# Performance work log

Measured on AMD Instinct MI355X. Metric: run time of the kernel, lower is better.

## Reference

```python
import jax, jax.numpy as jnp
import numpy as np

CH = 16        # channel_n
HID = 128      # hidden_size
IN_CH = 3      # input_channels (locked each step)
FIRE_RATE = 0.5


def _dwconv3x3(x, w, b):
    # depthwise 3x3, reflect padding (torch padding_mode='reflect', padding=1)
    xp = jnp.pad(x, ((0, 0), (0, 0), (1, 1), (1, 1)), mode='reflect')
    y = jax.lax.conv_general_dilated(
        xp, w, window_strides=(1, 1), padding='VALID',
        dimension_numbers=('NCHW', 'OIHW', 'NCHW'), feature_group_count=CH)
    return y + b[None, :, None, None]


def _conv1x1(x, w, b=None):
    # w: (out_ch, in_ch) -- squeezed 1x1 conv kernel
    y = jnp.einsum('bchw,oc->bohw', x, w)
    return y if b is None else y + b[None, :, None, None]


def setup_inputs() -> dict:
    key = jax.random.key(0)
    ks = jax.random.split(key, 8)
    B, H, W = 4, 256, 256
    x = jax.random.normal(ks[0], (B, CH, H, W), dtype=jnp.float32)
    # depthwise kernels: (CH, 1, 3, 3)
    p0_w = jax.random.normal(ks[1], (CH, 1, 3, 3), dtype=jnp.float32) * (1.0 / 3.0)
    p0_b = jax.random.normal(ks[2], (CH,), dtype=jnp.float32) * 0.1
    p1_w = jax.random.normal(ks[3], (CH, 1, 3, 3), dtype=jnp.float32) * (1.0 / 3.0)
    p1_b = jax.random.normal(ks[4], (CH,), dtype=jnp.float32) * 0.1
    # fc0: Conv2d(3*CH -> HID, k=1); fc1: Conv2d(HID -> CH, k=1, bias=False)
    fc0_w = jax.random.normal(ks[5], (HID, 3 * CH), dtype=jnp.float32) * (1.0 / np.sqrt(3 * CH))
    fc0_b = jax.random.normal(ks[6], (HID,), dtype=jnp.float32) * 0.1
    # NOTE: torch zero-inits fc1; we use small random weights so the reference is non-trivial.
    fc1_w = jax.random.normal(ks[7], (CH, HID), dtype=jnp.float32) * (0.1 / np.sqrt(HID))
    return {"x": x, "p0_w": p0_w, "p0_b": p0_b, "p1_w": p1_w, "p1_b": p1_b,
            "fc0_w": fc0_w, "fc0_b": fc0_b, "fc1_w": fc1_w, "steps": 32}


def reference(x, p0_w, p0_b, p1_w, p1_b, fc0_w, fc0_b, fc1_w, steps):
    B, _, H, W = x.shape
    input_image = x[:, :IN_CH]  # clone of input channels, re-written each step
    keys = jax.random.split(jax.random.key(42), steps)

    @jax.checkpoint
    def step(x, key):
        # perceive: depthwise 3x3 x2, concat with state
        z1 = _dwconv3x3(x, p0_w, p0_b)
        z2 = _dwconv3x3(x, p1_w, p1_b)
        y = jnp.concatenate([x, z1, z2], axis=1)        # [B, 3*CH, H, W]
        # 1x1-conv MLP
        dx = jax.nn.relu(_conv1x1(y, fc0_w, fc0_b))      # [B, HID, H, W]
        dx = _conv1x1(dx, fc1_w)                         # [B, CH, H, W]
        # stochastic fire mask: rand > fire_rate, broadcast over channels
        mask = (jax.random.uniform(key, (B, 1, H, W), dtype=x.dtype) > FIRE_RATE).astype(x.dtype)
        x = x + dx * mask                                # residual update
        x = x.at[:, :IN_CH].set(input_image)             # channel lock
        return x, None

    x, _ = jax.lax.scan(step, x, keys)
    out = x[:, 3]  # segmentation channel
    return out, x
```

## Files before the change

### kernel.cpp

```cpp
#include <hip/hip_runtime.h>
#include <cstdint>

#define CH     16
#define HPIX   256
#define WPIX   256
#define BATCH  4
#define HID    128
#define STEPS  32
#define PLANE  (HPIX * WPIX)
#define MASK_N (BATCH * PLANE)

#define TW 32
#define TH 8
#define XTW 34
#define XTH 10
#define NPX (XTH * XTW)
#define HSF 20

typedef _Float16 half8  __attribute__((ext_vector_type(8)));
typedef _Float16 half4e __attribute__((ext_vector_type(4)));
typedef float floatx4  __attribute__((ext_vector_type(4)));
typedef float floatx16 __attribute__((ext_vector_type(16)));

__host__ __device__ static inline void tf2x32(uint32_t k0, uint32_t k1,
                                              uint32_t x0, uint32_t x1,
                                              uint32_t& o0, uint32_t& o1) {
  const uint32_t ks2 = k0 ^ k1 ^ 0x1BD11BDAu;
#define TFROT(a) { x0 += x1; x1 = (x1 << (a)) | (x1 >> (32 - (a))); x1 ^= x0; }
  x0 += k0;  x1 += k1;
  TFROT(13) TFROT(15) TFROT(26) TFROT(6)
  x0 += k1;  x1 += ks2 + 1u;
  TFROT(17) TFROT(29) TFROT(16) TFROT(24)
  x0 += ks2; x1 += k0 + 2u;
  TFROT(13) TFROT(15) TFROT(26) TFROT(6)
  x0 += k0;  x1 += k1 + 3u;
  TFROT(17) TFROT(29) TFROT(16) TFROT(24)
  x0 += k1;  x1 += ks2 + 4u;
  TFROT(13) TFROT(15) TFROT(26) TFROT(6)
  x0 += ks2; x1 += k0 + 5u;
#undef TFROT
  o0 = x0; o1 = x1;
}

__global__ __launch_bounds__(256) void prep_weights(
    const float* __restrict__ fc0_w, const float* __restrict__ fc0_b,
    const float* __restrict__ fc1_w,
    const float* __restrict__ p0_w, const float* __restrict__ p0_b,
    const float* __restrict__ p1_w, const float* __restrict__ p1_b,
    _Float16* __restrict__ Mh, _Float16* __restrict__ W1h,
    float* __restrict__ bp) {
  const int idx = blockIdx.x * 256 + threadIdx.x;
  if (idx < 9 * HID * CH) {
    const int tap = idx / (HID * CH);
    const int rem = idx - tap * (HID * CH);
    const int h = rem >> 4, c = rem & 15;
    float m = fc0_w[h * 48 + 16 + c] * p0_w[c * 9 + tap]
            + fc0_w[h * 48 + 32 + c] * p1_w[c * 9 + tap];
    if (tap == 4) m += fc0_w[h * 48 + c];
    Mh[(tap * HID + h) * CH + c] = (_Float16)m;
  } else if (idx < 9 * HID * CH + CH * HID) {
    const int i2 = idx - 9 * HID * CH;
    W1h[i2] = (_Float16)fc1_w[i2];
  } else if (idx < 9 * HID * CH + CH * HID + HID) {
    const int h = idx - (9 * HID * CH + CH * HID);
    float s = fc0_b[h];
    for (int c = 0; c < CH; ++c)
      s += fc0_w[h * 48 + 16 + c] * p0_b[c]
         + fc0_w[h * 48 + 32 + c] * p1_b[c];
    bp[h] = s;
  }
}

__global__ __launch_bounds__(256) void nca_step(
    const float* __restrict__ x_in, float* __restrict__ x_out,
    const float* __restrict__ x0,
    const _Float16* __restrict__ Mh, const _Float16* __restrict__ W1h,
    const float* __restrict__ bp,
    uint32_t k0, uint32_t k1, int wrgb, float* __restrict__ outp) {
  __shared__ __align__(16) _Float16 halo[NPX * HSF];
  __shared__ __align__(16) _Float16 Hbuf[64 * HID];
  __shared__ float maskbuf[TW * TH];

  const int tid = threadIdx.x;
  const int w0 = blockIdx.x * TW;
  const int h0 = blockIdx.y * TH;
  const int b  = blockIdx.z;

  const int wv   = tid >> 6;
  const int lane = tid & 63;
  const int n    = lane & 15;
  const int g    = lane >> 4;
  const int c32  = lane & 31;
  const int q2   = lane >> 5;

  const float* __restrict__ xb  = x_in + (size_t)b * CH * PLANE;
  const float* __restrict__ x0b = x0   + (size_t)b * CH * PLANE;

  half8 Atap[9];
  #pragma unroll
  for (int t = 0; t < 9; ++t)
    Atap[t] = *(const half8*)(Mh + ((t * HID + 32 * wv + c32) << 4) + 8 * q2);
  half8 bw1[4];
  #pragma unroll
  for (int s = 0; s < 4; ++s)
    bw1[s] = *(const half8*)(W1h + n * HID + 32 * s + 8 * g);
  float4 bias4[4];
  #pragma unroll
  for (int rb = 0; rb < 4; ++rb)
    bias4[rb] = *(const float4*)(bp + 32 * wv + 8 * rb + 4 * q2);

  float4 xcv[4];
  size_t xoff[4];
  #pragma unroll
  for (int k = 0; k < 4; ++k) {
    xoff[k] = (size_t)n * PLANE
            + (size_t)(h0 + 2 * k + (wv >> 1)) * WPIX
            + w0 + 16 * (wv & 1) + 4 * g;
    xcv[k] = *(const float4*)(((n < 3) ? x0b : xb) + xoff[k]);
  }

  for (int t = tid; t < NPX; t += 256) {
    const int hr = t / XTW, hc = t - (t / XTW) * XTW;
    int gh = h0 + hr - 1;
    gh = (gh < 0) ? -gh : ((gh > HPIX - 1) ? (2 * (HPIX - 1) - gh) : gh);
    int gw = w0 + hc - 1;
    gw = (gw < 0) ? -gw : ((gw > WPIX - 1) ? (2 * (WPIX - 1) - gw) : gw);
    const float* __restrict__ srcS = xb  + gh * WPIX + gw;
    const float* __restrict__ src0 = x0b + gh * WPIX + gw;
    #pragma unroll
    for (int blk = 0; blk < 4; ++blk) {
      half4e h4;
      #pragma unroll
      for (int e = 0; e < 4; ++e) {
        const int c = 4 * blk + e;
        h4[e] = (_Float16)((c < 3 ? src0 : srcS)[(size_t)c * PLANE]);
      }
      *(half4e*)(halo + t * HSF + 4 * blk) = h4;
    }
  }

  {
    const int hp = h0 + (tid >> 5), wp = w0 + (tid & 31);
    const uint32_t j = (uint32_t)(b * PLANE + hp * WPIX + wp);
    uint32_t r0, r1;
    tf2x32(k0, k1, 0u, j, r0, r1);
    const uint32_t bits = r0 ^ r1;
    union { uint32_t i; float f; } cvt;
    cvt.i = (bits >> 9) | 0x3F800000u;
    maskbuf[tid] = ((cvt.f - 1.0f) > 0.5f) ? 1.0f : 0.0f;
  }
  __syncthreads();

  float* __restrict__ xob = x_out + (size_t)b * CH * PLANE;

  #pragma unroll
  for (int k = 0; k < 4; ++k) {
    #pragma unroll
    for (int cti = 0; cti < 2; ++cti) {
      const int ct = 2 * k + cti;
      half8 btap[9];
      #pragma unroll
      for (int dr = 0; dr < 3; ++dr) {
        #pragma unroll
        for (int dj = 0; dj < 3; ++dj) {
          const _Float16* hp =
              halo + ((ct + dr) * XTW + c32 + dj) * HSF + 8 * q2;
          const half4e lo = *(const half4e*)hp;
          const half4e hi = *(const half4e*)(hp + 4);
          half8 ff;
          ff[0] = lo[0]; ff[1] = lo[1]; ff[2] = lo[2]; ff[3] = lo[3];
          ff[4] = hi[0]; ff[5] = hi[1]; ff[6] = hi[2]; ff[7] = hi[3];
          btap[dr * 3 + dj] = ff;
        }
      }
      floatx16 acc = {0.f,0.f,0.f,0.f,0.f,0.f,0.f,0.f,
                      0.f,0.f,0.f,0.f,0.f,0.f,0.f,0.f};
      #pragma unroll
      for (int t = 0; t < 9; ++t)
        acc = __builtin_amdgcn_mfma_f32_32x32x16_f16(Atap[t], btap[t], acc,
                                                     0, 0, 0);
      const int ph  = 32 * cti + c32;
      const int n16 = c32 & 15;
      #pragma unroll
      for (int rb = 0; rb < 4; ++rb) {
        half4e hv;
        hv[0] = (_Float16)fmaxf(acc[4 * rb + 0] + bias4[rb].x, 0.f);
        hv[1] = (_Float16)fmaxf(acc[4 * rb + 1] + bias4[rb].y, 0.f);
        hv[2] = (_Float16)fmaxf(acc[4 * rb + 2] + bias4[rb].z, 0.f);
        hv[3] = (_Float16)fmaxf(acc[4 * rb + 3] + bias4[rb].w, 0.f);
        *(half4e*)(Hbuf + ph * HID + (((4 * wv + rb) ^ n16) << 3) + 4 * q2) = hv;
      }
    }
    __syncthreads();

    {
      floatx4 c2 = {0.f, 0.f, 0.f, 0.f};
      #pragma unroll
      for (int ks = 0; ks < 4; ++ks) {
        const half8 a2 = *(const half8*)(
            Hbuf + (16 * wv + n) * HID + (((4 * ks + g) ^ n) << 3));
        c2 = __builtin_amdgcn_mfma_f32_16x16x32_f16(a2, bw1[ks], c2, 0, 0, 0);
      }
      const int prow = 2 * k + (wv >> 1);
      const int pcol = 16 * (wv & 1) + 4 * g;
      const float4 mk = *(const float4*)(maskbuf + prow * TW + pcol);
      const float4 xc = xcv[k];
      float4 res;
      res.x = (n < 3) ? xc.x : fmaf(mk.x, c2[0], xc.x);
      res.y = (n < 3) ? xc.y : fmaf(mk.y, c2[1], xc.y);
      res.z = (n < 3) ? xc.z : fmaf(mk.z, c2[2], xc.z);
      res.w = (n < 3) ? xc.w : fmaf(mk.w, c2[3], xc.w);
      if (n >= 3 || wrgb)
        *(float4*)(xob + xoff[k]) = res;
      if (wrgb && n == 3) {
        *(float4*)(outp + (size_t)b * PLANE
                   + (size_t)(h0 + prow) * WPIX + w0 + pcol) = res;
      }
    }
    if (k < 3) __syncthreads();
  }
}

extern "C" void kernel_launch(void* const* d_in, const int* in_sizes, int n_in,
                              void* d_out, int out_size, void* d_ws, size_t ws_size,
                              hipStream_t stream) {
  const float* x     = (const float*)d_in[0];
  const float* p0_w  = (const float*)d_in[1];
  const float* p0_b  = (const float*)d_in[2];
  const float* p1_w  = (const float*)d_in[3];
  const float* p1_b  = (const float*)d_in[4];
  const float* fc0_w = (const float*)d_in[5];
  const float* fc0_b = (const float*)d_in[6];
  const float* fc1_w = (const float*)d_in[7];

  uint32_t kk[STEPS][2];
  for (int i = 0; i < STEPS; ++i) {
    uint32_t a, b2;
    tf2x32(0u, 42u, 0u, (uint32_t)i, a, b2);
    kk[i][0] = a;
    kk[i][1] = b2;
  }

  float* out = (float*)d_out;
  float* bufA = out + MASK_N;
  float* bufB = (float*)d_ws;

  _Float16* Mh  = (_Float16*)((char*)d_ws + ((size_t)32 << 20));
  _Float16* W1h = Mh + 9 * HID * CH;
  float*    bpr = (float*)((char*)W1h + CH * HID * 2);

  const int prep_n = 9 * HID * CH + CH * HID + HID;
  prep_weights<<<dim3((prep_n + 255) / 256), dim3(256), 0, stream>>>(
      fc0_w, fc0_b, fc1_w, p0_w, p0_b, p1_w, p1_b, Mh, W1h, bpr);

  const dim3 grid(WPIX / TW, HPIX / TH, BATCH);
  const dim3 block(256);

  for (int i = 0; i < STEPS; ++i) {
    const float* src = (i == 0) ? x : ((i & 1) ? bufB : bufA);
    float* dst = (i & 1) ? bufA : bufB;
    nca_step<<<grid, block, 0, stream>>>(src, dst, x, Mh, W1h, bpr,
                                         kk[i][0], kk[i][1],
                                         (i == STEPS - 1) ? 1 : 0, out);
  }
}
```

Before: 759.4 us.

## Fuse two NCA steps per launch using halo recomputation

Each kernel launch now advances two NCA steps. It loads a 2-pixel halo frame, computes the step-1 update for the interior tile and also recomputes it on a 1-pixel rim, then runs step 2 from shared memory. The tile width is halved to 16, and reflect-padding fixups are applied at image borders. This halves the number of launches and the global memory round trips of the state. In exchange it adds redundant rim computation of about 52 extra pixels per 128, more barriers, and more shared memory.

```diff
diff --git a/kernel.cpp b/kernel.cpp
--- a/kernel.cpp
+++ b/kernel.cpp
@@ -7,15 +7,17 @@
 #define BATCH  4
 #define HID    128
 #define STEPS  32
+#define NPAIR  (STEPS / 2)
 #define PLANE  (HPIX * WPIX)
 #define MASK_N (BATCH * PLANE)
 
-#define TW 32
+#define TW 16
 #define TH 8
-#define XTW 34
-#define XTH 10
-#define NPX (XTH * XTW)
+#define F_W 20
+#define F_H 12
+#define FRAME_PX (F_W * F_H)
 #define HSF 20
+#define RIM_N 52
 
 typedef _Float16 half8  __attribute__((ext_vector_type(8)));
 typedef _Float16 half4e __attribute__((ext_vector_type(4)));
@@ -40,6 +42,25 @@
   x0 += ks2; x1 += k0 + 5u;
 #undef TFROT
   o0 = x0; o1 = x1;
+}
+
+__device__ __forceinline__ float tf_bit(uint32_t k0, uint32_t k1, uint32_t j) {
+  uint32_t r0, r1;
+  tf2x32(k0, k1, 0u, j, r0, r1);
+  const uint32_t bits = r0 ^ r1;
+  union { uint32_t i; float f; } cvt;
+  cvt.i = (bits >> 9) | 0x3F800000u;
+  return ((cvt.f - 1.0f) > 0.5f) ? 1.0f : 0.0f;
+}
+
+__device__ __forceinline__ int refl(int v) {
+  return v < 0 ? -v : (v > HPIX - 1 ? 2 * (HPIX - 1) - v : v);
+}
+
+__device__ __forceinline__ void rim_rc(int slot, int& r, int& c) {
+  if (slot < 18)      { r = 0; c = slot; }
+  else if (slot < 36) { r = 9; c = slot - 18; }
+  else { const int u = slot - 36; r = 1 + (u >> 1); c = (u & 1) * 17; }
 }
 
 __global__ __launch_bounds__(256) void prep_weights(
@@ -71,15 +92,56 @@
   }
 }
 
-__global__ __launch_bounds__(256) void nca_step(
+#define GEMM1_TILE(SRC, FR0, FC0, ACC)                                        \
+  { _Pragma("unroll") for (int dr = 0; dr < 3; ++dr) {                        \
+      _Pragma("unroll") for (int dj = 0; dj < 3; ++dj) {                      \
+        const _Float16* hp = (SRC)                                            \
+            + (((FR0) + dr) * F_W + (FC0) + dj) * HSF + 8 * q2;               \
+        const half4e lo = *(const half4e*)hp;                                 \
+        const half4e hi = *(const half4e*)(hp + 4);                           \
+        half8 ff;                                                             \
+        ff[0] = lo[0]; ff[1] = lo[1]; ff[2] = lo[2]; ff[3] = lo[3];           \
+        ff[4] = hi[0]; ff[5] = hi[1]; ff[6] = hi[2]; ff[7] = hi[3];           \
+        ACC = __builtin_amdgcn_mfma_f32_32x32x16_f16(Atap[dr * 3 + dj], ff,   \
+                                                     ACC, 0, 0, 0);           \
+      } } }
+
+#define HBUF_WRITE(PH, ACC)                                                   \
+  { const int n16 = c32 & 15;                                                 \
+    _Pragma("unroll") for (int rb = 0; rb < 4; ++rb) {                        \
+      half4e hv;                                                              \
+      hv[0] = (_Float16)fmaxf(ACC[4 * rb + 0] + bias4[rb].x, 0.f);            \
+      hv[1] = (_Float16)fmaxf(ACC[4 * rb + 1] + bias4[rb].y, 0.f);            \
+      hv[2] = (_Float16)fmaxf(ACC[4 * rb + 2] + bias4[rb].z, 0.f);            \
+      hv[3] = (_Float16)fmaxf(ACC[4 * rb + 3] + bias4[rb].w, 0.f);            \
+      *(half4e*)(Hbuf + (PH) * HID + (((4 * wv + rb) ^ n16) << 3) + 4 * q2)   \
+          = hv; } }
+
+#define GEMM2_C2(C2)                                                          \
+  { _Pragma("unroll") for (int ks2 = 0; ks2 < 4; ++ks2) {                     \
+      const half8 a2 = *(const half8*)(                                       \
+          Hbuf + (16 * wv + n) * HID + (((4 * ks2 + g) ^ n) << 3));           \
+      C2 = __builtin_amdgcn_mfma_f32_16x16x32_f16(a2, bw1[ks2], C2, 0, 0, 0); \
+    } }
+
+#define CPY_PX(DI, SI)                                                        \
+  { uint2* dp = (uint2*)(halo2 + (DI));                                       \
+    const uint2* sp = (const uint2*)(halo2 + (SI));                           \
+    dp[0] = sp[0]; dp[1] = sp[1]; dp[2] = sp[2]; dp[3] = sp[3]; }
+
+__global__ __launch_bounds__(256, 4) void nca_step2(
     const float* __restrict__ x_in, float* __restrict__ x_out,
     const float* __restrict__ x0,
     const _Float16* __restrict__ Mh, const _Float16* __restrict__ W1h,
     const float* __restrict__ bp,
-    uint32_t k0, uint32_t k1, int wrgb, float* __restrict__ outp) {
-  __shared__ __align__(16) _Float16 halo[NPX * HSF];
+    uint32_t k0a, uint32_t k1a, uint32_t k0b, uint32_t k1b,
+    int wrgb, float* __restrict__ outp) {
+  __shared__ __align__(16) _Float16 halo1[FRAME_PX * HSF];
+  __shared__ __align__(16) _Float16 halo2[FRAME_PX * HSF];
   __shared__ __align__(16) _Float16 Hbuf[64 * HID];
-  __shared__ float maskbuf[TW * TH];
+  __shared__ __align__(16) float mask1o[128];
+  __shared__ __align__(16) float mask2o[128];
+  __shared__ __align__(16) float mask1r[64];
 
   const int tid = threadIdx.x;
   const int w0 = blockIdx.x * TW;
@@ -95,6 +157,7 @@
 
   const float* __restrict__ xb  = x_in + (size_t)b * CH * PLANE;
   const float* __restrict__ x0b = x0   + (size_t)b * CH * PLANE;
+  float* __restrict__ xob = x_out + (size_t)b * CH * PLANE;
 
   half8 Atap[9];
   #pragma unroll
@@ -109,22 +172,31 @@
   for (int rb = 0; rb < 4; ++rb)
     bias4[rb] = *(const float4*)(bp + 32 * wv + 8 * rb + 4 * q2);
 
-  float4 xcv[4];
-  size_t xoff[4];
-  #pragma unroll
-  for (int k = 0; k < 4; ++k) {
-    xoff[k] = (size_t)n * PLANE
-            + (size_t)(h0 + 2 * k + (wv >> 1)) * WPIX
-            + w0 + 16 * (wv & 1) + 4 * g;
-    xcv[k] = *(const float4*)(((n < 3) ? x0b : xb) + xoff[k]);
-  }
-
-  for (int t = tid; t < NPX; t += 256) {
-    const int hr = t / XTW, hc = t - (t / XTW) * XTW;
-    int gh = h0 + hr - 1;
-    gh = (gh < 0) ? -gh : ((gh > HPIX - 1) ? (2 * (HPIX - 1) - gh) : gh);
-    int gw = w0 + hc - 1;
-    gw = (gw < 0) ? -gw : ((gw > WPIX - 1) ? (2 * (WPIX - 1) - gw) : gw);
+  size_t xoff[2];
+  float4 xcv[2];
+  #pragma unroll
+  for (int hf = 0; hf < 2; ++hf) {
+    xoff[hf] = (size_t)n * PLANE
+             + (size_t)(h0 + 4 * hf + wv) * WPIX + w0 + 4 * g;
+    xcv[hf] = *(const float4*)(((n < 3) ? x0b : xb) + xoff[hf]);
+  }
+
+  if (tid < 128) {
+    const int tr = tid >> 4, tc = tid & 15;
+    const uint32_t j = (uint32_t)(b * PLANE + (h0 + tr) * WPIX + (w0 + tc));
+    mask1o[tid] = tf_bit(k0a, k1a, j);
+    mask2o[tid] = tf_bit(k0b, k1b, j);
+  } else if (tid < 128 + RIM_N) {
+    int r, c;
+    rim_rc(tid - 128, r, c);
+    const int gy = refl(h0 + r - 1), gx = refl(w0 + c - 1);
+    const uint32_t j = (uint32_t)(b * PLANE + gy * WPIX + gx);
+    mask1r[tid - 128] = tf_bit(k0a, k1a, j);
+  }
+
+  if (tid < FRAME_PX) {
+    const int fr = tid / F_W, fc = tid - (tid / F_W) * F_W;
+    const int gh = refl(h0 + fr - 2), gw = refl(w0 + fc - 2);
     const float* __restrict__ srcS = xb  + gh * WPIX + gw;
     const float* __restrict__ src0 = x0b + gh * WPIX + gw;
     #pragma unroll
@@ -135,89 +207,121 @@
         const int c = 4 * blk + e;
         h4[e] = (_Float16)((c < 3 ? src0 : srcS)[(size_t)c * PLANE]);
       }
-      *(half4e*)(halo + t * HSF + 4 * blk) = h4;
-    }
-  }
-
-  {
-    const int hp = h0 + (tid >> 5), wp = w0 + (tid & 31);
-    const uint32_t j = (uint32_t)(b * PLANE + hp * WPIX + wp);
-    uint32_t r0, r1;
-    tf2x32(k0, k1, 0u, j, r0, r1);
-    const uint32_t bits = r0 ^ r1;
-    union { uint32_t i; float f; } cvt;
-    cvt.i = (bits >> 9) | 0x3F800000u;
-    maskbuf[tid] = ((cvt.f - 1.0f) > 0.5f) ? 1.0f : 0.0f;
+      *(half4e*)(halo1 + tid * HSF + 4 * blk) = h4;
+    }
   }
   __syncthreads();
 
-  float* __restrict__ xob = x_out + (size_t)b * CH * PLANE;
-
-  #pragma unroll
-  for (int k = 0; k < 4; ++k) {
+  #pragma unroll
+  for (int hf = 0; hf < 2; ++hf) {
     #pragma unroll
     for (int cti = 0; cti < 2; ++cti) {
-      const int ct = 2 * k + cti;
-      half8 btap[9];
-      #pragma unroll
-      for (int dr = 0; dr < 3; ++dr) {
-        #pragma unroll
-        for (int dj = 0; dj < 3; ++dj) {
-          const _Float16* hp =
-              halo + ((ct + dr) * XTW + c32 + dj) * HSF + 8 * q2;
-          const half4e lo = *(const half4e*)hp;
-          const half4e hi = *(const half4e*)(hp + 4);
-          half8 ff;
-          ff[0] = lo[0]; ff[1] = lo[1]; ff[2] = lo[2]; ff[3] = lo[3];
-          ff[4] = hi[0]; ff[5] = hi[1]; ff[6] = hi[2]; ff[7] = hi[3];
-          btap[dr * 3 + dj] = ff;
-        }
-      }
+      const int ct = 2 * hf + cti;
+      const int prow = 2 * ct + (c32 >> 4), pcol = c32 & 15;
       floatx16 acc = {0.f,0.f,0.f,0.f,0.f,0.f,0.f,0.f,
                       0.f,0.f,0.f,0.f,0.f,0.f,0.f,0.f};
-      #pragma unroll
-      for (int t = 0; t < 9; ++t)
-        acc = __builtin_amdgcn_mfma_f32_32x32x16_f16(Atap[t], btap[t], acc,
-                                                     0, 0, 0);
-      const int ph  = 32 * cti + c32;
-      const int n16 = c32 & 15;
-      #pragma unroll
-      for (int rb = 0; rb < 4; ++rb) {
-        half4e hv;
-        hv[0] = (_Float16)fmaxf(acc[4 * rb + 0] + bias4[rb].x, 0.f);
-        hv[1] = (_Float16)fmaxf(acc[4 * rb + 1] + bias4[rb].y, 0.f);
-        hv[2] = (_Float16)fmaxf(acc[4 * rb + 2] + bias4[rb].z, 0.f);
-        hv[3] = (_Float16)fmaxf(acc[4 * rb + 3] + bias4[rb].w, 0.f);
-        *(half4e*)(Hbuf + ph * HID + (((4 * wv + rb) ^ n16) << 3) + 4 * q2) = hv;
+      GEMM1_TILE(halo1, prow + 1, pcol + 1, acc);
+      HBUF_WRITE(32 * cti + c32, acc);
+    }
+    __syncthreads();
+    floatx4 c2 = {0.f, 0.f, 0.f, 0.f};
+    GEMM2_C2(c2);
+    const int ct2 = 4 * hf + wv;
+    const float4 mk = *(const float4*)(mask1o + ct2 * 16 + 4 * g);
+    const float4 xc = xcv[hf];
+    float4 res;
+    res.x = (n < 3) ? xc.x : fmaf(mk.x, c2[0], xc.x);
+    res.y = (n < 3) ? xc.y : fmaf(mk.y, c2[1], xc.y);
+    res.z = (n < 3) ? xc.z : fmaf(mk.z, c2[2], xc.z);
+    res.w = (n < 3) ? xc.w : fmaf(mk.w, c2[3], xc.w);
+    xcv[hf] = res;
+    {
+      const int base = ((ct2 + 2) * F_W + (4 * g + 2)) * HSF + n;
+      halo2[base          ] = (_Float16)res.x;
+      halo2[base + HSF    ] = (_Float16)res.y;
+      halo2[base + 2 * HSF] = (_Float16)res.z;
+      halo2[base + 3 * HSF] = (_Float16)res.w;
+    }
+    __syncthreads();
+  }
+
+  {
+    int rr[4], rc_[4];
+    float xcr[4];
+    #pragma unroll
+    for (int e = 0; e < 4; ++e) {
+      const int sl = 16 * wv + 4 * g + e;
+      int r, c;
+      rim_rc(sl < RIM_N ? sl : RIM_N - 1, r, c);
+      rr[e] = r; rc_[e] = c;
+      const int gy = refl(h0 + r - 1), gx = refl(w0 + c - 1);
+      xcr[e] = ((n < 3) ? x0b : xb)[(size_t)n * PLANE + gy * WPIX + gx];
+    }
+    #pragma unroll
+    for (int cti = 0; cti < 2; ++cti) {
+      int sl1 = 32 * cti + c32;
+      if (sl1 >= RIM_N) sl1 = RIM_N - 1;
+      int r1, c1;
+      rim_rc(sl1, r1, c1);
+      floatx16 acc = {0.f,0.f,0.f,0.f,0.f,0.f,0.f,0.f,
+                      0.f,0.f,0.f,0.f,0.f,0.f,0.f,0.f};
+      GEMM1_TILE(halo1, r1, c1, acc);
+      HBUF_WRITE(32 * cti + c32, acc);
+    }
+    __syncthreads();
+    floatx4 c2 = {0.f, 0.f, 0.f, 0.f};
+    GEMM2_C2(c2);
+    const float4 mk = *(const float4*)(mask1r + 16 * wv + 4 * g);
+    const float mka[4] = {mk.x, mk.y, mk.z, mk.w};
+    #pragma unroll
+    for (int e = 0; e < 4; ++e) {
+      if (16 * wv + 4 * g + e < RIM_N) {
+        const float rv = (n < 3) ? xcr[e] : fmaf(mka[e], c2[e], xcr[e]);
+        halo2[((rr[e] + 1) * F_W + (rc_[e] + 1)) * HSF + n] = (_Float16)rv;
       }
     }
     __syncthreads();
-
-    {
-      floatx4 c2 = {0.f, 0.f, 0.f, 0.f};
-      #pragma unroll
-      for (int ks = 0; ks < 4; ++ks) {
-        const half8 a2 = *(const half8*)(
-            Hbuf + (16 * wv + n) * HID + (((4 * ks + g) ^ n) << 3));
-        c2 = __builtin_amdgcn_mfma_f32_16x16x32_f16(a2, bw1[ks], c2, 0, 0, 0);
-      }
-      const int prow = 2 * k + (wv >> 1);
-      const int pcol = 16 * (wv & 1) + 4 * g;
-      const float4 mk = *(const float4*)(maskbuf + prow * TW + pcol);
-      const float4 xc = xcv[k];
-      float4 res;
-      res.x = (n < 3) ? xc.x : fmaf(mk.x, c2[0], xc.x);
-      res.y = (n < 3) ? xc.y : fmaf(mk.y, c2[1], xc.y);
-      res.z = (n < 3) ? xc.z : fmaf(mk.z, c2[2], xc.z);
-      res.w = (n < 3) ? xc.w : fmaf(mk.w, c2[3], xc.w);
-      if (n >= 3 || wrgb)
-        *(float4*)(xob + xoff[k]) = res;
-      if (wrgb && n == 3) {
-        *(float4*)(outp + (size_t)b * PLANE
-                   + (size_t)(h0 + prow) * WPIX + w0 + pcol) = res;
-      }
-    }
-    if (k < 3) __syncthreads();
+  }
+
+  if (h0 == 0 && tid < 18)
+    CPY_PX((1 * F_W + 1 + tid) * HSF, (3 * F_W + 1 + tid) * HSF);
+  if (h0 == HPIX - TH && tid < 18)
+    CPY_PX((10 * F_W + 1 + tid) * HSF, (8 * F_W + 1 + tid) * HSF);
+  __syncthreads();
+  if (w0 == 0 && tid < 10)
+    CPY_PX(((1 + tid) * F_W + 1) * HSF, ((1 + tid) * F_W + 3) * HSF);
+  if (w0 == WPIX - TW && tid < 10)
+    CPY_PX(((1 + tid) * F_W + 18) * HSF, ((1 + tid) * F_W + 16) * HSF);
+  __syncthreads();
+
+  #pragma unroll
+  for (int hf = 0; hf < 2; ++hf) {
+    #pragma unroll
+    for (int cti = 0; cti < 2; ++cti) {
+      const int ct = 2 * hf + cti;
+      const int prow = 2 * ct + (c32 >> 4), pcol = c32 & 15;
+      floatx16 acc = {0.f,0.f,0.f,0.f,0.f,0.f,0.f,0.f,
+                      0.f,0.f,0.f,0.f,0.f,0.f,0.f,0.f};
+      GEMM1_TILE(halo2, prow + 1, pcol + 1, acc);
+      HBUF_WRITE(32 * cti + c32, acc);
+    }
+    __syncthreads();
+    floatx4 c2 = {0.f, 0.f, 0.f, 0.f};
+    GEMM2_C2(c2);
+    const int ct2 = 4 * hf + wv;
+    const float4 mk = *(const float4*)(mask2o + ct2 * 16 + 4 * g);
+    const float4 xc = xcv[hf];
+    float4 res;
+    res.x = (n < 3) ? xc.x : fmaf(mk.x, c2[0], xc.x);
+    res.y = (n < 3) ? xc.y : fmaf(mk.y, c2[1], xc.y);
+    res.z = (n < 3) ? xc.z : fmaf(mk.z, c2[2], xc.z);
+    res.w = (n < 3) ? xc.w : fmaf(mk.w, c2[3], xc.w);
+    if (n >= 3 || wrgb)
+      *(float4*)(xob + xoff[hf]) = res;
+    if (wrgb && n == 3)
+      *(float4*)(outp + (size_t)b * PLANE
+                 + (size_t)(h0 + ct2) * WPIX + w0 + 4 * g) = res;
+    if (hf == 0) __syncthreads();
   }
 }
 
@@ -241,7 +345,7 @@
     kk[i][1] = b2;
   }
 
-  float* out = (float*)d_out;
+  float* out  = (float*)d_out;
   float* bufA = out + MASK_N;
   float* bufB = (float*)d_ws;
 
@@ -256,11 +360,12 @@
   const dim3 grid(WPIX / TW, HPIX / TH, BATCH);
   const dim3 block(256);
 
-  for (int i = 0; i < STEPS; ++i) {
-    const float* src = (i == 0) ? x : ((i & 1) ? bufB : bufA);
-    float* dst = (i & 1) ? bufA : bufB;
-    nca_step<<<grid, block, 0, stream>>>(src, dst, x, Mh, W1h, bpr,
-                                         kk[i][0], kk[i][1],
-                                         (i == STEPS - 1) ? 1 : 0, out);
-  }
-}
+  for (int j = 0; j < NPAIR; ++j) {
+    const float* src = (j == 0) ? x : ((j & 1) ? bufB : bufA);
+    float* dst = (j & 1) ? bufA : bufB;
+    nca_step2<<<grid, block, 0, stream>>>(src, dst, x, Mh, W1h, bpr,
+                                          kk[2 * j][0], kk[2 * j][1],
+                                          kk[2 * j + 1][0], kk[2 * j + 1][1],
+                                          (j == NPAIR - 1) ? 1 : 0, out);
+  }
+}
```

Result: slower. 1.141 ms (+50.2%).
